# Kernel optimization log

Measured on AMD Instinct MI355X. Metric: run time of the kernel, lower is better.

Reference implementation:

```python
import jax, jax.numpy as jnp
import numpy as np

D_MODEL = 1024
N_HEADS = 16
D_K = D_MODEL // N_HEADS
NEG_INF = -1e9  # large negative instead of -inf for numerical/grad safety


def setup_inputs() -> dict:
    key = jax.random.key(0)
    ks = jax.random.split(key, 12)
    B, N = 2, 2048
    s = 1.0 / np.sqrt(D_MODEL)
    return {
        "Q_src": jax.random.normal(ks[0], (B, N, D_MODEL), jnp.float32),
        "K_src": jax.random.normal(ks[1], (B, N, D_MODEL), jnp.float32),
        "V_src": jax.random.normal(ks[2], (B, N, D_MODEL), jnp.float32),
        "value_weights": jax.random.uniform(ks[3], (B, N), jnp.float32),
        "mask": jnp.ones((B, N), dtype=bool),
        "Wq_w": jax.random.normal(ks[4], (D_MODEL, D_MODEL), jnp.float32) * s,
        "Wq_b": jnp.zeros((D_MODEL,), jnp.float32),
        "Wk_w": jax.random.normal(ks[5], (D_MODEL, D_MODEL), jnp.float32) * s,
        "Wk_b": jnp.zeros((D_MODEL,), jnp.float32),
        "Wv_w": jax.random.normal(ks[6], (D_MODEL, D_MODEL), jnp.float32) * s,
        "Wv_b": jnp.zeros((D_MODEL,), jnp.float32),
        "out_w": jax.random.normal(ks[7], (D_MODEL, D_MODEL), jnp.float32) * s,
        "out_b": jnp.zeros((D_MODEL,), jnp.float32),
    }


def _split(x):
    # [B, N, D] -> [B, H, N, d_k]
    B, N, D = x.shape
    return x.reshape(B, N, N_HEADS, D_K).transpose(0, 2, 1, 3)


def reference(Q_src, K_src, V_src, value_weights, mask,
              Wq_w, Wq_b, Wk_w, Wk_b, Wv_w, Wv_b, out_w, out_b):
    # torch Linear convention: y = x @ W^T + b
    Q = _split(Q_src @ Wq_w.T + Wq_b)   # [B,H,Nq,dk]
    K = _split(K_src @ Wk_w.T + Wk_b)   # [B,H,Nk,dk]
    V = _split(V_src @ Wv_w.T + Wv_b)   # [B,H,Nk,dk]

    scores = jnp.einsum('bhqd,bhkd->bhqk', Q, K) / jnp.sqrt(jnp.asarray(D_K, Q.dtype))
    scores = jnp.where(mask[:, None, None, :], scores, NEG_INF)
    attn = jax.nn.softmax(scores, axis=-1)

    Vw = V * value_weights[:, None, :, None]
    context = jnp.einsum('bhqk,bhkd->bhqd', attn, Vw)  # [B,H,Nq,dk]
    B, H, Nq, dk = context.shape
    context = context.transpose(0, 2, 1, 3).reshape(B, Nq, H * dk)
    return context @ out_w.T + out_b
```

## Files before the change

### kernel.cpp

```cpp
#include <hip/hip_runtime.h>
#include <hip/hip_bf16.h>


typedef __attribute__((ext_vector_type(8))) short short8;
typedef __attribute__((ext_vector_type(4))) float f32x4;

#define MFMA16(a, b, c) __builtin_amdgcn_mfma_f32_16x16x32_bf16((a), (b), (c), 0, 0, 0)

static __device__ __forceinline__ unsigned short f2b(float f) {
  unsigned int u = __float_as_uint(f);
  u += 0x7fffu + ((u >> 16) & 1u);
  return (unsigned short)(u >> 16);
}

static __device__ __forceinline__ unsigned int pkbf2(float lo, float hi) {
  union { __hip_bfloat162 h2; unsigned int u; } c;
  c.h2 = __float22bfloat162_rn(float2{lo, hi});
  return c.u;
}

static __device__ __forceinline__ void load_lds16(const void* g, void* s) {
  __builtin_amdgcn_global_load_lds((__attribute__((address_space(1))) void*)g,
                                   (__attribute__((address_space(3))) void*)s, 16, 0, 0);
}

struct CvtArgs {
  const float* s[7];
  unsigned short* d[7];
  int n8[7];
};

__global__ void cvt_all_kernel(CvtArgs a) {
  const int y = blockIdx.y;
  const float* __restrict__ src = a.s[y];
  unsigned short* __restrict__ dst = a.d[y];
  const int n8 = a.n8[y];
  int i = blockIdx.x * blockDim.x + threadIdx.x;
  const int stride = gridDim.x * blockDim.x;
  for (; i < n8; i += stride) {
    float4 va = ((const float4*)src)[2 * i];
    float4 vb = ((const float4*)src)[2 * i + 1];
    short8 o;
    o[0] = (short)f2b(va.x); o[1] = (short)f2b(va.y);
    o[2] = (short)f2b(va.z); o[3] = (short)f2b(va.w);
    o[4] = (short)f2b(vb.x); o[5] = (short)f2b(vb.y);
    o[6] = (short)f2b(vb.z); o[7] = (short)f2b(vb.w);
    ((short8*)dst)[i] = o;
  }
}

struct ProjArgs {
  const unsigned short* A[3];
  const unsigned short* B[3];
  unsigned short* Cb[3];
  const float* bias[3];
  float scale[3];
  const float* vw;
};

__global__ __launch_bounds__(256, 3) void gemm_proj(ProjArgs p) {
  __shared__ unsigned char Ash[128 * 128];
  __shared__ unsigned char Bsh[128 * 128];
  const int z = blockIdx.z;
  const unsigned short* __restrict__ A = p.A[z];
  const unsigned short* __restrict__ B = p.B[z];
  unsigned short* __restrict__ Cb = p.Cb[z];
  const float* __restrict__ bias = p.bias[z];
  const float* __restrict__ vw = p.vw;
  const float oscale = p.scale[z];
  const int N = 1024, K = 1024;

  const int tid = threadIdx.x;
  const int l = tid & 63, w = tid >> 6;
  const int wr = w >> 1, wc = w & 1;
  const int hh = l >> 4, q15 = l & 15;
  const int m0 = blockIdx.x * 128, n0 = blockIdx.y * 128;

  const f32x4 fzero = {0.f, 0.f, 0.f, 0.f};
  f32x4 acc[4][4];
#pragma unroll
  for (int i = 0; i < 4; ++i)
#pragma unroll
    for (int j = 0; j < 4; ++j) acc[i][j] = fzero;

  const int lr8 = l >> 3;
  const int scolb = (l & 7) ^ (lr8 & 7);
  const unsigned short* Ag = A + (long)(m0 + w * 32 + lr8) * K + scolb * 8;
  const unsigned short* Bg = B + (long)(n0 + w * 32 + lr8) * K + scolb * 8;

  for (int kk = 0; kk < K; kk += 64) {
#pragma unroll
    for (int c = 0; c < 4; ++c)
      load_lds16(Ag + (long)(c * 8) * K + kk, Ash + (w * 32 + c * 8) * 128);
#pragma unroll
    for (int c = 0; c < 4; ++c)
      load_lds16(Bg + (long)(c * 8) * K + kk, Bsh + (w * 32 + c * 8) * 128);
    __syncthreads();

#pragma unroll
    for (int k0 = 0; k0 < 2; ++k0) {
      short8 af[4], bf_[4];
#pragma unroll
      for (int mt = 0; mt < 4; ++mt) {
        const int ra = wr * 64 + mt * 16 + q15;
        af[mt] = *(const short8*)(Ash + ra * 128 + (((k0 * 4 + hh) ^ (ra & 7)) << 4));
      }
#pragma unroll
      for (int nt = 0; nt < 4; ++nt) {
        const int rb = wc * 64 + nt * 16 + q15;
        bf_[nt] = *(const short8*)(Bsh + rb * 128 + (((k0 * 4 + hh) ^ (rb & 7)) << 4));
      }
#pragma unroll
      for (int mt = 0; mt < 4; ++mt)
#pragma unroll
        for (int nt = 0; nt < 4; ++nt)
          acc[mt][nt] = MFMA16(af[mt], bf_[nt], acc[mt][nt]);
    }
    __syncthreads();
  }

#pragma unroll
  for (int mt = 0; mt < 4; ++mt) {
#pragma unroll
    for (int j = 0; j < 4; ++j) {
      const int row = m0 + wr * 64 + mt * 16 + hh * 4 + j;
      float vwv = 1.f;
      if (z == 2) vwv = vw[row];
#pragma unroll
      for (int nt = 0; nt < 4; ++nt) {
        const int col = n0 + wc * 64 + nt * 16 + q15;
        float v = acc[mt][nt][j] + bias[col];
        if (z != 2) {
          Cb[(long)row * N + col] = f2b(v * oscale);
        } else {
          v *= vwv;
          const int bb = row >> 11, nseq = row & 2047;
          const int hcol = col >> 6, dc = col & 63;
          const int n5 = nseq & 31;
          const int np = (nseq & ~31) | (((n5 >> 2) & 3) << 3) | ((n5 >> 4) << 2) | (n5 & 3);
          Cb[((long)((bb * 16 + hcol) * 64 + dc)) * 2048 + np] = f2b(v);
        }
      }
    }
  }
}

__global__ __launch_bounds__(256, 3) void gemm_out64(
    const unsigned short* __restrict__ A, const unsigned short* __restrict__ B,
    float* __restrict__ Cf, const float* __restrict__ bias) {
  const int N = 1024, K = 1024;
  const int tid = threadIdx.x;
  const int l = tid & 63, w = tid >> 6;
  const int m0 = blockIdx.x * 128, n0 = blockIdx.y * 64;
  __shared__ unsigned char Ash[2][128 * 128];
  __shared__ unsigned char Bsh[2][64 * 128];

  const f32x4 fzero = {0.f, 0.f, 0.f, 0.f};
  f32x4 acc[2][4];
#pragma unroll
  for (int i = 0; i < 2; ++i)
#pragma unroll
    for (int j = 0; j < 4; ++j) acc[i][j] = fzero;

  const int lr8 = l >> 3;
  const int scolb = (l & 7) ^ (lr8 & 7);
  const unsigned short* Ag = A + (long)(m0 + w * 32 + lr8) * K + scolb * 8;
  const unsigned short* Bg = B + (long)(n0 + w * 16 + lr8) * K + scolb * 8;

  auto stage = [&](int kk, int buf) {
#pragma unroll
    for (int c = 0; c < 4; ++c)
      load_lds16(Ag + (long)(c * 8) * K + kk, Ash[buf] + (w * 32 + c * 8) * 128);
#pragma unroll
    for (int c = 0; c < 2; ++c)
      load_lds16(Bg + (long)(c * 8) * K + kk, Bsh[buf] + (w * 16 + c * 8) * 128);
  };

  stage(0, 0);
  int cur = 0;
  for (int kk = 0; kk < K; kk += 64) {
    if (kk + 64 < K) {
      stage(kk + 64, cur ^ 1);
      asm volatile("s_waitcnt vmcnt(6)" ::: "memory");
    } else {
      asm volatile("s_waitcnt vmcnt(0)" ::: "memory");
    }
    __builtin_amdgcn_s_barrier();

    const unsigned char* Ab = Ash[cur];
    const unsigned char* Bb = Bsh[cur];
    short8 af[2][2], bf_[2][4];
#pragma unroll
    for (int k0 = 0; k0 < 2; ++k0) {
#pragma unroll
      for (int mt = 0; mt < 2; ++mt) {
        const int ra = w * 32 + mt * 16 + (l & 15);
        af[k0][mt] = *(const short8*)(Ab + ra * 128 + (((k0 * 4 + (l >> 4)) ^ (ra & 7)) << 4));
      }
#pragma unroll
      for (int nt = 0; nt < 4; ++nt) {
        const int rb = nt * 16 + (l & 15);
        bf_[k0][nt] = *(const short8*)(Bb + rb * 128 + (((k0 * 4 + (l >> 4)) ^ (rb & 7)) << 4));
      }
    }
#pragma unroll
    for (int k0 = 0; k0 < 2; ++k0)
#pragma unroll
      for (int mt = 0; mt < 2; ++mt)
#pragma unroll
        for (int nt = 0; nt < 4; ++nt)
          acc[mt][nt] = MFMA16(af[k0][mt], bf_[k0][nt], acc[mt][nt]);

    asm volatile("s_waitcnt lgkmcnt(0)" ::: "memory");
    __builtin_amdgcn_s_barrier();
    cur ^= 1;
  }

#pragma unroll
  for (int mt = 0; mt < 2; ++mt)
#pragma unroll
    for (int j = 0; j < 4; ++j) {
      const int row = m0 + w * 32 + mt * 16 + (l >> 4) * 4 + j;
#pragma unroll
      for (int nt = 0; nt < 4; ++nt) {
        const int col = n0 + nt * 16 + (l & 15);
        Cf[(long)row * N + col] = acc[mt][nt][j] + bias[col];
      }
    }
}

__global__ __launch_bounds__(512, 4) void flash_attn(
    const unsigned short* __restrict__ Qp, const unsigned short* __restrict__ Kp,
    const unsigned short* __restrict__ Vt, unsigned short* __restrict__ Ctx) {
  const int tid = threadIdx.x, l = tid & 63, w = tid >> 6;
  const int set = w >> 2, w4 = w & 3;
  const int kvbase = set << 10;
  const int q0 = blockIdx.x * 128;
  const int bh = blockIdx.y, b = bh >> 4, h = bh & 15;
  const int hh = l >> 4;
  const int q15 = l & 15;

  __shared__ unsigned char Lds[81920];
  unsigned char* base = Lds + set * 40960;
  unsigned char* k0 = base;
  unsigned char* k1 = base + 8192;
  unsigned char* vr = base + 16384;
  unsigned char* vn = base + 24576;
  unsigned char* vw_ = base + 32768;

  short8 qfA[2], qfB[2];
  {
    const unsigned short* qa =
        Qp + (long)(b * 2048 + q0 + w4 * 32 + q15) * 1024 + h * 64 + hh * 8;
    qfA[0] = *(const short8*)qa;
    qfA[1] = *(const short8*)(qa + 32);
    const unsigned short* qb = qa + 16 * 1024;
    qfB[0] = *(const short8*)qb;
    qfB[1] = *(const short8*)(qb + 32);
  }

  const f32x4 fzero = {0.f, 0.f, 0.f, 0.f};
  f32x4 accA[4], accB[4];
#pragma unroll
  for (int i = 0; i < 4; ++i) { accA[i] = fzero; accB[i] = fzero; }
  f32x4 accLA = fzero, accLB = fzero;

  const short one_bf = (short)0x3F80;
  const short8 ones8 = {one_bf, one_bf, one_bf, one_bf, one_bf, one_bf, one_bf, one_bf};

  const int lr8 = l >> 3;
  const int scolb = (l & 7) ^ (lr8 & 7);
  const unsigned short* Kg =
      Kp + (long)(b * 2048 + kvbase + w4 * 16 + lr8) * 1024 + h * 64 + scolb * 8;
  const unsigned short* Vg =
      Vt + (long)(bh * 64 + w4 * 16 + lr8) * 2048 + kvbase + scolb * 8;

  auto stageK = [&](int kv0, unsigned char* dst) {
#pragma unroll
    for (int c = 0; c < 2; ++c)
      load_lds16(Kg + (long)(kv0 + c * 8) * 1024, dst + (w4 * 16 + c * 8) * 128);
  };
  auto stageV = [&](int kv0, unsigned char* dst) {
#pragma unroll
    for (int c = 0; c < 2; ++c)
      load_lds16(Vg + (long)(c * 8) * 2048 + kv0, dst + (w4 * 16 + c * 8) * 128);
  };

  auto qkt2 = [&](const unsigned char* Kb, f32x4* sA, f32x4* sB) {
#pragma unroll
    for (int nt = 0; nt < 4; ++nt) {
      const int rk = nt * 16 + q15;
      short8 kf0 = *(const short8*)(Kb + rk * 128 + ((hh ^ (rk & 7)) << 4));
      short8 kf1 = *(const short8*)(Kb + rk * 128 + (((4 + hh) ^ (rk & 7)) << 4));
      f32x4 za = fzero, zb = fzero;
      za = MFMA16(kf0, qfA[0], za);
      zb = MFMA16(kf0, qfB[0], zb);
      za = MFMA16(kf1, qfA[1], za);
      zb = MFMA16(kf1, qfB[1], zb);
      sA[nt] = za;
      sB[nt] = zb;
    }
  };

  union S8 { short8 s8; unsigned int u[4]; };
  S8 paA1, paA2, paB1, paB2;

  auto softmax = [&](f32x4* s, S8& p1, S8& p2) {
    float p[4][4];
#pragma unroll
    for (int nt = 0; nt < 4; ++nt)
#pragma unroll
      for (int j = 0; j < 4; ++j)
        p[nt][j] = __builtin_amdgcn_exp2f(s[nt][j]);
    p1.u[0] = pkbf2(p[0][0], p[0][1]); p1.u[1] = pkbf2(p[0][2], p[0][3]);
    p1.u[2] = pkbf2(p[1][0], p[1][1]); p1.u[3] = pkbf2(p[1][2], p[1][3]);
    p2.u[0] = pkbf2(p[2][0], p[2][1]); p2.u[1] = pkbf2(p[2][2], p[2][3]);
    p2.u[2] = pkbf2(p[3][0], p[3][1]); p2.u[3] = pkbf2(p[3][2], p[3][3]);
  };

  stageK(0, k0);  stageV(0, vr);
  stageK(64, k1); stageV(64, vn);
  asm volatile("s_waitcnt vmcnt(4)" ::: "memory");
  __builtin_amdgcn_s_barrier();

  {
    f32x4 sA[4], sB[4];
    qkt2(k0, sA, sB);
    softmax(sA, paA1, paA2);
    softmax(sB, paB1, paB2);
  }
  asm volatile("s_waitcnt lgkmcnt(0)" ::: "memory");

  for (int t = 0; t < 15; ++t) {
    asm volatile("s_waitcnt vmcnt(0)" ::: "memory");
    __builtin_amdgcn_s_barrier();
    if (t < 14) {
      stageK((t + 2) * 64, (t & 1) ? k1 : k0);
      stageV((t + 2) * 64, vw_);
    }

    const unsigned char* kb = (t & 1) ? k0 : k1;
    f32x4 sA[4], sB[4];
    qkt2(kb, sA, sB);

#pragma unroll
    for (int dt = 0; dt < 4; ++dt) {
      const int rv = dt * 16 + q15;
      const unsigned char* vrow = vr + rv * 128;
      const int sw = rv & 7;
      short8 vf0 = *(const short8*)(vrow + ((hh ^ sw) << 4));
      short8 vf1 = *(const short8*)(vrow + (((4 + hh) ^ sw) << 4));
      accA[dt] = MFMA16(paA1.s8, vf0, accA[dt]);
      accB[dt] = MFMA16(paB1.s8, vf0, accB[dt]);
      accA[dt] = MFMA16(paA2.s8, vf1, accA[dt]);
      accB[dt] = MFMA16(paB2.s8, vf1, accB[dt]);
    }
    accLA = MFMA16(paA1.s8, ones8, accLA);
    accLA = MFMA16(paA2.s8, ones8, accLA);
    accLB = MFMA16(paB1.s8, ones8, accLB);
    accLB = MFMA16(paB2.s8, ones8, accLB);

    softmax(sA, paA1, paA2);
    softmax(sB, paB1, paB2);

    asm volatile("s_waitcnt lgkmcnt(0)" ::: "memory");
    unsigned char* tmp = vr; vr = vn; vn = vw_; vw_ = tmp;
  }

#pragma unroll
  for (int dt = 0; dt < 4; ++dt) {
    const int rv = dt * 16 + q15;
    const unsigned char* vrow = vr + rv * 128;
    const int sw = rv & 7;
    short8 vf0 = *(const short8*)(vrow + ((hh ^ sw) << 4));
    short8 vf1 = *(const short8*)(vrow + (((4 + hh) ^ sw) << 4));
    accA[dt] = MFMA16(paA1.s8, vf0, accA[dt]);
    accB[dt] = MFMA16(paB1.s8, vf0, accB[dt]);
    accA[dt] = MFMA16(paA2.s8, vf1, accA[dt]);
    accB[dt] = MFMA16(paB2.s8, vf1, accB[dt]);
  }
  accLA = MFMA16(paA1.s8, ones8, accLA);
  accLA = MFMA16(paA2.s8, ones8, accLA);
  accLB = MFMA16(paB1.s8, ones8, accLB);
  accLB = MFMA16(paB2.s8, ones8, accLB);

  __syncthreads();
  f32x4* cb = (f32x4*)Lds;
  f32x4* lb = (f32x4*)(Lds + 32768);
  if (set == 1) {
#pragma unroll
    for (int g = 0; g < 2; ++g) {
#pragma unroll
      for (int dt = 0; dt < 4; ++dt)
        cb[(w4 * 8 + g * 4 + dt) * 64 + l] = g ? accB[dt] : accA[dt];
      lb[(w4 * 2 + g) * 64 + l] = g ? accLB : accLA;
    }
  }
  __syncthreads();
  if (set == 0) {
#pragma unroll
    for (int g = 0; g < 2; ++g) {
      f32x4* acc = g ? accB : accA;
      f32x4 aL = g ? accLB : accLA;
      aL += lb[(w4 * 2 + g) * 64 + l];
      f32x4 inv;
#pragma unroll
      for (int j = 0; j < 4; ++j) inv[j] = 1.f / aL[j];
#pragma unroll
      for (int dt = 0; dt < 4; ++dt) {
        f32x4 a = acc[dt] + cb[(w4 * 8 + g * 4 + dt) * 64 + l];
#pragma unroll
        for (int j = 0; j < 4; ++j) {
          const int row = b * 2048 + q0 + w4 * 32 + g * 16 + hh * 4 + j;
          const int col = h * 64 + dt * 16 + q15;
          Ctx[(long)row * 1024 + col] = f2b(a[j] * inv[j]);
        }
      }
    }
  }
}

extern "C" void kernel_launch(void* const* d_in, const int* in_sizes, int n_in,
                              void* d_out, int out_size, void* d_ws, size_t ws_size,
                              hipStream_t stream) {
  const float* Qs = (const float*)d_in[0];
  const float* Ks = (const float*)d_in[1];
  const float* Vs = (const float*)d_in[2];
  const float* vw = (const float*)d_in[3];
  const float* Wq = (const float*)d_in[5];
  const float* Wqb = (const float*)d_in[6];
  const float* Wk = (const float*)d_in[7];
  const float* Wkb = (const float*)d_in[8];
  const float* Wv = (const float*)d_in[9];
  const float* Wvb = (const float*)d_in[10];
  const float* Wo = (const float*)d_in[11];
  const float* Wob = (const float*)d_in[12];
  float* out = (float*)d_out;

  char* ws = (char*)d_ws;
  const size_t MB = 1024 * 1024;
  unsigned short* Qsb = (unsigned short*)(ws + 0 * MB);
  unsigned short* Ksb = (unsigned short*)(ws + 8 * MB);
  unsigned short* Vsb = (unsigned short*)(ws + 16 * MB);
  unsigned short* Wq16 = (unsigned short*)(ws + 24 * MB);
  unsigned short* Wk16 = (unsigned short*)(ws + 26 * MB);
  unsigned short* Wv16 = (unsigned short*)(ws + 28 * MB);
  unsigned short* Wo16 = (unsigned short*)(ws + 30 * MB);
  unsigned short* Qp = (unsigned short*)(ws + 32 * MB);
  unsigned short* Kp = (unsigned short*)(ws + 40 * MB);
  unsigned short* Vt = (unsigned short*)(ws + 48 * MB);
  unsigned short* Ctx = (unsigned short*)(ws + 56 * MB);

  CvtArgs ca;
  ca.s[0] = Qs;  ca.d[0] = Qsb;  ca.n8[0] = 4096 * 1024 / 8;
  ca.s[1] = Ks;  ca.d[1] = Ksb;  ca.n8[1] = 4096 * 1024 / 8;
  ca.s[2] = Vs;  ca.d[2] = Vsb;  ca.n8[2] = 4096 * 1024 / 8;
  ca.s[3] = Wq;  ca.d[3] = Wq16; ca.n8[3] = 1024 * 1024 / 8;
  ca.s[4] = Wk;  ca.d[4] = Wk16; ca.n8[4] = 1024 * 1024 / 8;
  ca.s[5] = Wv;  ca.d[5] = Wv16; ca.n8[5] = 1024 * 1024 / 8;
  ca.s[6] = Wo;  ca.d[6] = Wo16; ca.n8[6] = 1024 * 1024 / 8;
  cvt_all_kernel<<<dim3(1024, 7), 256, 0, stream>>>(ca);

  ProjArgs pa;
  pa.A[0] = Qsb;  pa.B[0] = Wq16; pa.Cb[0] = Qp; pa.bias[0] = Wqb;
  pa.A[1] = Ksb;  pa.B[1] = Wk16; pa.Cb[1] = Kp; pa.bias[1] = Wkb;
  pa.A[2] = Vsb;  pa.B[2] = Wv16; pa.Cb[2] = Vt; pa.bias[2] = Wvb;
  pa.scale[0] = 0.18033688011112042f;
  pa.scale[1] = 1.f;
  pa.scale[2] = 1.f;
  pa.vw = vw;
  gemm_proj<<<dim3(32, 8, 3), 256, 0, stream>>>(pa);

  flash_attn<<<dim3(16, 32), 512, 0, stream>>>(Qp, Kp, Vt, Ctx);

  gemm_out64<<<dim3(32, 16), 256, 0, stream>>>(Ctx, Wo16, out, Wob);
}
```

Before: 118.0 us.

## Fuse fp32-to-bf16 activation conversion into projection GEMM and remap blocks per XCD

The projection GEMM now reads fp32 Q/K/V sources directly into registers, converts them to bf16 and writes them to LDS, with the next tile's loads prefetched and explicit waitcnt/barrier sync. This removes the separate conversion pass over the large activations and its bf16 round-trip through memory; only the weights are still pre-converted. Separately, the projection, attention and output kernels remap block indices so that blocks landing on the same XCD share A-rows or heads, which is meant to improve L2 locality. The cost is doubled fp32 global read width for A inside the GEMM and more register pressure from the prefetch buffers.

Result: faster. 108.8 us, median of 2 (-7.8%).

```diff
diff --git a/kernel.cpp b/kernel.cpp
--- a/kernel.cpp
+++ b/kernel.cpp
@@ -25,32 +25,26 @@
 }
 
 struct CvtArgs {
-  const float* s[7];
-  unsigned short* d[7];
-  int n8[7];
+  const float* s[4];
+  unsigned short* d[4];
 };
 
-__global__ void cvt_all_kernel(CvtArgs a) {
-  const int y = blockIdx.y;
-  const float* __restrict__ src = a.s[y];
-  unsigned short* __restrict__ dst = a.d[y];
-  const int n8 = a.n8[y];
-  int i = blockIdx.x * blockDim.x + threadIdx.x;
-  const int stride = gridDim.x * blockDim.x;
-  for (; i < n8; i += stride) {
-    float4 va = ((const float4*)src)[2 * i];
-    float4 vb = ((const float4*)src)[2 * i + 1];
-    short8 o;
-    o[0] = (short)f2b(va.x); o[1] = (short)f2b(va.y);
-    o[2] = (short)f2b(va.z); o[3] = (short)f2b(va.w);
-    o[4] = (short)f2b(vb.x); o[5] = (short)f2b(vb.y);
-    o[6] = (short)f2b(vb.z); o[7] = (short)f2b(vb.w);
-    ((short8*)dst)[i] = o;
-  }
+__global__ void cvt_w_kernel(CvtArgs a) {
+  const float* __restrict__ src = a.s[blockIdx.y];
+  unsigned short* __restrict__ dst = a.d[blockIdx.y];
+  const int i = blockIdx.x * blockDim.x + threadIdx.x;
+  float4 va = ((const float4*)src)[2 * i];
+  float4 vb = ((const float4*)src)[2 * i + 1];
+  short8 o;
+  o[0] = (short)f2b(va.x); o[1] = (short)f2b(va.y);
+  o[2] = (short)f2b(va.z); o[3] = (short)f2b(va.w);
+  o[4] = (short)f2b(vb.x); o[5] = (short)f2b(vb.y);
+  o[6] = (short)f2b(vb.z); o[7] = (short)f2b(vb.w);
+  ((short8*)dst)[i] = o;
 }
 
 struct ProjArgs {
-  const unsigned short* A[3];
+  const float* A32[3];
   const unsigned short* B[3];
   unsigned short* Cb[3];
   const float* bias[3];
@@ -61,8 +55,16 @@
 __global__ __launch_bounds__(256, 3) void gemm_proj(ProjArgs p) {
   __shared__ unsigned char Ash[128 * 128];
   __shared__ unsigned char Bsh[128 * 128];
-  const int z = blockIdx.z;
-  const unsigned short* __restrict__ A = p.A[z];
+
+  const int P = blockIdx.x + (blockIdx.y << 5) + (blockIdx.z << 8);
+  const int xcd = P & 7;
+  const int t = P >> 3;
+  const int by = t & 7;
+  const int g = t >> 3;
+  const int bx = xcd + ((g & 3) << 3);
+  const int z = g >> 2;
+
+  const float* __restrict__ A32 = p.A32[z];
   const unsigned short* __restrict__ B = p.B[z];
   unsigned short* __restrict__ Cb = p.Cb[z];
   const float* __restrict__ bias = p.bias[z];
@@ -74,7 +76,7 @@
   const int l = tid & 63, w = tid >> 6;
   const int wr = w >> 1, wc = w & 1;
   const int hh = l >> 4, q15 = l & 15;
-  const int m0 = blockIdx.x * 128, n0 = blockIdx.y * 128;
+  const int m0 = bx * 128, n0 = by * 128;
 
   const f32x4 fzero = {0.f, 0.f, 0.f, 0.f};
   f32x4 acc[4][4];
@@ -85,17 +87,42 @@
 
   const int lr8 = l >> 3;
   const int scolb = (l & 7) ^ (lr8 & 7);
-  const unsigned short* Ag = A + (long)(m0 + w * 32 + lr8) * K + scolb * 8;
+  const float* Ag32 = A32 + (long)(m0 + w * 32 + lr8) * K + scolb * 8;
   const unsigned short* Bg = B + (long)(n0 + w * 32 + lr8) * K + scolb * 8;
 
+  float4 a4[4][2];
+  auto loadA = [&](int kk) {
+#pragma unroll
+    for (int c = 0; c < 4; ++c) {
+      const float* src = Ag32 + (long)(c * 8) * K + kk;
+      a4[c][0] = *(const float4*)(src);
+      a4[c][1] = *(const float4*)(src + 4);
+    }
+  };
+
+  loadA(0);
   for (int kk = 0; kk < K; kk += 64) {
 #pragma unroll
-    for (int c = 0; c < 4; ++c)
-      load_lds16(Ag + (long)(c * 8) * K + kk, Ash + (w * 32 + c * 8) * 128);
+    for (int c = 0; c < 4; ++c) {
+      union { short8 s8; unsigned int u[4]; } v;
+      v.u[0] = pkbf2(a4[c][0].x, a4[c][0].y);
+      v.u[1] = pkbf2(a4[c][0].z, a4[c][0].w);
+      v.u[2] = pkbf2(a4[c][1].x, a4[c][1].y);
+      v.u[3] = pkbf2(a4[c][1].z, a4[c][1].w);
+      *(short8*)(Ash + (w * 32 + c * 8 + lr8) * 128 + (l & 7) * 16) = v.s8;
+    }
 #pragma unroll
     for (int c = 0; c < 4; ++c)
       load_lds16(Bg + (long)(c * 8) * K + kk, Bsh + (w * 32 + c * 8) * 128);
-    __syncthreads();
+    asm volatile("" ::: "memory");
+    if (kk + 64 < K) {
+      loadA(kk + 64);
+      asm volatile("s_waitcnt vmcnt(8)" ::: "memory");
+    } else {
+      asm volatile("s_waitcnt vmcnt(0)" ::: "memory");
+    }
+    asm volatile("s_waitcnt lgkmcnt(0)" ::: "memory");
+    __builtin_amdgcn_s_barrier();
 
 #pragma unroll
     for (int k0 = 0; k0 < 2; ++k0) {
@@ -116,7 +143,8 @@
         for (int nt = 0; nt < 4; ++nt)
           acc[mt][nt] = MFMA16(af[mt], bf_[nt], acc[mt][nt]);
     }
-    __syncthreads();
+    asm volatile("s_waitcnt lgkmcnt(0)" ::: "memory");
+    __builtin_amdgcn_s_barrier();
   }
 
 #pragma unroll
@@ -151,7 +179,14 @@
   const int N = 1024, K = 1024;
   const int tid = threadIdx.x;
   const int l = tid & 63, w = tid >> 6;
-  const int m0 = blockIdx.x * 128, n0 = blockIdx.y * 64;
+
+  const int P = blockIdx.x + (blockIdx.y << 5);
+  const int xcd = P & 7;
+  const int t = P >> 3;
+  const int ny = t & 15;
+  const int bx = xcd + ((t >> 4) << 3);
+  const int m0 = bx * 128, n0 = ny * 64;
+
   __shared__ unsigned char Ash[2][128 * 128];
   __shared__ unsigned char Bsh[2][64 * 128];
 
@@ -235,8 +270,14 @@
   const int tid = threadIdx.x, l = tid & 63, w = tid >> 6;
   const int set = w >> 2, w4 = w & 3;
   const int kvbase = set << 10;
-  const int q0 = blockIdx.x * 128;
-  const int bh = blockIdx.y, b = bh >> 4, h = bh & 15;
+
+  const int P = blockIdx.x + (blockIdx.y << 4);
+  const int xcd = P & 7;
+  const int t = P >> 3;
+  const int qb = t & 15;
+  const int bh = xcd + ((t >> 4) << 3);
+  const int q0 = qb * 128;
+  const int b = bh >> 4, h = bh & 15;
   const int hh = l >> 4;
   const int q15 = l & 15;
 
@@ -254,9 +295,9 @@
         Qp + (long)(b * 2048 + q0 + w4 * 32 + q15) * 1024 + h * 64 + hh * 8;
     qfA[0] = *(const short8*)qa;
     qfA[1] = *(const short8*)(qa + 32);
-    const unsigned short* qb = qa + 16 * 1024;
-    qfB[0] = *(const short8*)qb;
-    qfB[1] = *(const short8*)(qb + 32);
+    const unsigned short* qb_ = qa + 16 * 1024;
+    qfB[0] = *(const short8*)qb_;
+    qfB[1] = *(const short8*)(qb_ + 32);
   }
 
   const f32x4 fzero = {0.f, 0.f, 0.f, 0.f};
@@ -331,15 +372,15 @@
   }
   asm volatile("s_waitcnt lgkmcnt(0)" ::: "memory");
 
-  for (int t = 0; t < 15; ++t) {
+  for (int t2 = 0; t2 < 15; ++t2) {
     asm volatile("s_waitcnt vmcnt(0)" ::: "memory");
     __builtin_amdgcn_s_barrier();
-    if (t < 14) {
-      stageK((t + 2) * 64, (t & 1) ? k1 : k0);
-      stageV((t + 2) * 64, vw_);
-    }
-
-    const unsigned char* kb = (t & 1) ? k0 : k1;
+    if (t2 < 14) {
+      stageK((t2 + 2) * 64, (t2 & 1) ? k1 : k0);
+      stageV((t2 + 2) * 64, vw_);
+    }
+
+    const unsigned char* kb = (t2 & 1) ? k0 : k1;
     f32x4 sA[4], sB[4];
     qkt2(kb, sA, sB);
 
@@ -439,9 +480,6 @@
 
   char* ws = (char*)d_ws;
   const size_t MB = 1024 * 1024;
-  unsigned short* Qsb = (unsigned short*)(ws + 0 * MB);
-  unsigned short* Ksb = (unsigned short*)(ws + 8 * MB);
-  unsigned short* Vsb = (unsigned short*)(ws + 16 * MB);
   unsigned short* Wq16 = (unsigned short*)(ws + 24 * MB);
   unsigned short* Wk16 = (unsigned short*)(ws + 26 * MB);
   unsigned short* Wv16 = (unsigned short*)(ws + 28 * MB);
@@ -452,19 +490,16 @@
   unsigned short* Ctx = (unsigned short*)(ws + 56 * MB);
 
   CvtArgs ca;
-  ca.s[0] = Qs;  ca.d[0] = Qsb;  ca.n8[0] = 4096 * 1024 / 8;
-  ca.s[1] = Ks;  ca.d[1] = Ksb;  ca.n8[1] = 4096 * 1024 / 8;
-  ca.s[2] = Vs;  ca.d[2] = Vsb;  ca.n8[2] = 4096 * 1024 / 8;
-  ca.s[3] = Wq;  ca.d[3] = Wq16; ca.n8[3] = 1024 * 1024 / 8;
-  ca.s[4] = Wk;  ca.d[4] = Wk16; ca.n8[4] = 1024 * 1024 / 8;
-  ca.s[5] = Wv;  ca.d[5] = Wv16; ca.n8[5] = 1024 * 1024 / 8;
-  ca.s[6] = Wo;  ca.d[6] = Wo16; ca.n8[6] = 1024 * 1024 / 8;
-  cvt_all_kernel<<<dim3(1024, 7), 256, 0, stream>>>(ca);
+  ca.s[0] = Wq; ca.d[0] = Wq16;
+  ca.s[1] = Wk; ca.d[1] = Wk16;
+  ca.s[2] = Wv; ca.d[2] = Wv16;
+  ca.s[3] = Wo; ca.d[3] = Wo16;
+  cvt_w_kernel<<<dim3(512, 4), 256, 0, stream>>>(ca);
 
   ProjArgs pa;
-  pa.A[0] = Qsb;  pa.B[0] = Wq16; pa.Cb[0] = Qp; pa.bias[0] = Wqb;
-  pa.A[1] = Ksb;  pa.B[1] = Wk16; pa.Cb[1] = Kp; pa.bias[1] = Wkb;
-  pa.A[2] = Vsb;  pa.B[2] = Wv16; pa.Cb[2] = Vt; pa.bias[2] = Wvb;
+  pa.A32[0] = Qs;  pa.B[0] = Wq16; pa.Cb[0] = Qp; pa.bias[0] = Wqb;
+  pa.A32[1] = Ks;  pa.B[1] = Wk16; pa.Cb[1] = Kp; pa.bias[1] = Wkb;
+  pa.A32[2] = Vs;  pa.B[2] = Wv16; pa.Cb[2] = Vt; pa.bias[2] = Wvb;
   pa.scale[0] = 0.18033688011112042f;
   pa.scale[1] = 1.f;
   pa.scale[2] = 1.f;
```

## Remap block indices for XCD-aware L2 locality; load projection operands directly from global

Applied to the files above, without the earlier changes.

All three kernels remap the linear block id so that blocks placed round-robin on the same XCD share the same A rows or the same (batch, head), which should improve L2 reuse on the multi-die MI355X. The projection GEMM also drops LDS staging and barriers and loads MFMA fragments straight from global memory into registers. That removes the synchronization cost, but each wave now reads its operands from global with no sharing through LDS, which raises global and L2 traffic. The direct loads also use a less coalesced strided pattern.

After: 169.6 us. 43.8% more time.

```diff
diff --git a/kernel.cpp b/kernel.cpp
--- a/kernel.cpp
+++ b/kernel.cpp
@@ -59,9 +59,14 @@
 };
 
 __global__ __launch_bounds__(256, 3) void gemm_proj(ProjArgs p) {
-  __shared__ unsigned char Ash[128 * 128];
-  __shared__ unsigned char Bsh[128 * 128];
-  const int z = blockIdx.z;
+  const int P = blockIdx.x + (blockIdx.y << 5) + (blockIdx.z << 8);
+  const int xcd = P & 7;
+  const int t = P >> 3;
+  const int by = t & 7;
+  const int g = t >> 3;
+  const int bx = xcd + ((g & 3) << 3);
+  const int z = g >> 2;
+
   const unsigned short* __restrict__ A = p.A[z];
   const unsigned short* __restrict__ B = p.B[z];
   unsigned short* __restrict__ Cb = p.Cb[z];
@@ -74,7 +79,7 @@
   const int l = tid & 63, w = tid >> 6;
   const int wr = w >> 1, wc = w & 1;
   const int hh = l >> 4, q15 = l & 15;
-  const int m0 = blockIdx.x * 128, n0 = blockIdx.y * 128;
+  const int m0 = bx * 128, n0 = by * 128;
 
   const f32x4 fzero = {0.f, 0.f, 0.f, 0.f};
   f32x4 acc[4][4];
@@ -83,40 +88,28 @@
 #pragma unroll
     for (int j = 0; j < 4; ++j) acc[i][j] = fzero;
 
-  const int lr8 = l >> 3;
-  const int scolb = (l & 7) ^ (lr8 & 7);
-  const unsigned short* Ag = A + (long)(m0 + w * 32 + lr8) * K + scolb * 8;
-  const unsigned short* Bg = B + (long)(n0 + w * 32 + lr8) * K + scolb * 8;
+  const unsigned short* Ab = A + (long)(m0 + wr * 64 + q15) * K + hh * 8;
+  const unsigned short* Bb = B + (long)(n0 + wc * 64 + q15) * K + hh * 8;
 
   for (int kk = 0; kk < K; kk += 64) {
-#pragma unroll
-    for (int c = 0; c < 4; ++c)
-      load_lds16(Ag + (long)(c * 8) * K + kk, Ash + (w * 32 + c * 8) * 128);
-#pragma unroll
-    for (int c = 0; c < 4; ++c)
-      load_lds16(Bg + (long)(c * 8) * K + kk, Bsh + (w * 32 + c * 8) * 128);
-    __syncthreads();
-
-#pragma unroll
-    for (int k0 = 0; k0 < 2; ++k0) {
-      short8 af[4], bf_[4];
-#pragma unroll
-      for (int mt = 0; mt < 4; ++mt) {
-        const int ra = wr * 64 + mt * 16 + q15;
-        af[mt] = *(const short8*)(Ash + ra * 128 + (((k0 * 4 + hh) ^ (ra & 7)) << 4));
-      }
-#pragma unroll
-      for (int nt = 0; nt < 4; ++nt) {
-        const int rb = wc * 64 + nt * 16 + q15;
-        bf_[nt] = *(const short8*)(Bsh + rb * 128 + (((k0 * 4 + hh) ^ (rb & 7)) << 4));
-      }
+    short8 af[4][2], bf[4][2];
+#pragma unroll
+    for (int mt = 0; mt < 4; ++mt)
+#pragma unroll
+      for (int k0 = 0; k0 < 2; ++k0)
+        af[mt][k0] = *(const short8*)(Ab + (long)mt * 16 * K + kk + k0 * 32);
+#pragma unroll
+    for (int nt = 0; nt < 4; ++nt)
+#pragma unroll
+      for (int k0 = 0; k0 < 2; ++k0)
+        bf[nt][k0] = *(const short8*)(Bb + (long)nt * 16 * K + kk + k0 * 32);
+#pragma unroll
+    for (int k0 = 0; k0 < 2; ++k0)
 #pragma unroll
       for (int mt = 0; mt < 4; ++mt)
 #pragma unroll
         for (int nt = 0; nt < 4; ++nt)
-          acc[mt][nt] = MFMA16(af[mt], bf_[nt], acc[mt][nt]);
-    }
-    __syncthreads();
+          acc[mt][nt] = MFMA16(af[mt][k0], bf[nt][k0], acc[mt][nt]);
   }
 
 #pragma unroll
@@ -151,7 +144,14 @@
   const int N = 1024, K = 1024;
   const int tid = threadIdx.x;
   const int l = tid & 63, w = tid >> 6;
-  const int m0 = blockIdx.x * 128, n0 = blockIdx.y * 64;
+
+  const int P = blockIdx.x + (blockIdx.y << 5);
+  const int xcd = P & 7;
+  const int t = P >> 3;
+  const int ny = t & 15;
+  const int bx = xcd + ((t >> 4) << 3);
+  const int m0 = bx * 128, n0 = ny * 64;
+
   __shared__ unsigned char Ash[2][128 * 128];
   __shared__ unsigned char Bsh[2][64 * 128];
 
@@ -235,8 +235,14 @@
   const int tid = threadIdx.x, l = tid & 63, w = tid >> 6;
   const int set = w >> 2, w4 = w & 3;
   const int kvbase = set << 10;
-  const int q0 = blockIdx.x * 128;
-  const int bh = blockIdx.y, b = bh >> 4, h = bh & 15;
+
+  const int P = blockIdx.x + (blockIdx.y << 4);
+  const int xcd = P & 7;
+  const int t = P >> 3;
+  const int qb = t & 15;
+  const int bh = xcd + ((t >> 4) << 3);
+  const int q0 = qb * 128;
+  const int b = bh >> 4, h = bh & 15;
   const int hh = l >> 4;
   const int q15 = l & 15;
 
@@ -254,9 +260,9 @@
         Qp + (long)(b * 2048 + q0 + w4 * 32 + q15) * 1024 + h * 64 + hh * 8;
     qfA[0] = *(const short8*)qa;
     qfA[1] = *(const short8*)(qa + 32);
-    const unsigned short* qb = qa + 16 * 1024;
-    qfB[0] = *(const short8*)qb;
-    qfB[1] = *(const short8*)(qb + 32);
+    const unsigned short* qb_ = qa + 16 * 1024;
+    qfB[0] = *(const short8*)qb_;
+    qfB[1] = *(const short8*)(qb_ + 32);
   }
 
   const f32x4 fzero = {0.f, 0.f, 0.f, 0.f};
@@ -331,15 +337,15 @@
   }
   asm volatile("s_waitcnt lgkmcnt(0)" ::: "memory");
 
-  for (int t = 0; t < 15; ++t) {
+  for (int t2 = 0; t2 < 15; ++t2) {
     asm volatile("s_waitcnt vmcnt(0)" ::: "memory");
     __builtin_amdgcn_s_barrier();
-    if (t < 14) {
-      stageK((t + 2) * 64, (t & 1) ? k1 : k0);
-      stageV((t + 2) * 64, vw_);
-    }
-
-    const unsigned char* kb = (t & 1) ? k0 : k1;
+    if (t2 < 14) {
+      stageK((t2 + 2) * 64, (t2 & 1) ? k1 : k0);
+      stageV((t2 + 2) * 64, vw_);
+    }
+
+    const unsigned char* kb = (t2 & 1) ? k0 : k1;
     f32x4 sA[4], sB[4];
     qkt2(kb, sA, sB);
 
```
